# Optimization experiments

Measured on AMD Instinct MI355X. Metric: run time of the kernel, lower is better.

Reference implementation:

```python
import jax, jax.numpy as jnp
import numpy as np

EPS = 1e-7  # keras backend epsilon


def _tril_indices(stack_size: int) -> np.ndarray:
    # matches np.nonzero(np.tri(S, S, -1).ravel())[0] in build()
    return np.nonzero(np.tri(stack_size, stack_size, -1).ravel())[0]


def setup_inputs() -> dict:
    key = jax.random.key(0)
    x = jax.random.normal(key, (8, 512, 256), dtype=jnp.float32)
    return {"x": x}


def reference(x) -> jnp.ndarray:
    B, S, D = x.shape
    tril = jnp.asarray(_tril_indices(S))  # static, length S*(S-1)/2
    # pairwise squared L2 over feature dim: (B, S, S, D) -> (B, S, S)
    diff = x[:, :, None, :] - x[:, None, :, :]
    d2 = jnp.sum(jnp.square(diff), axis=-1)
    d = jnp.sqrt(jnp.maximum(d2, EPS))
    # flatten the S x S matrix and gather strict lower-triangular entries
    out = d.reshape(B, S * S)[:, tril]  # (B, S*(S-1)/2)
    return out
```

## Files before the change

### kernel.cpp

```cpp
#include <hip/hip_runtime.h>
#include <hip/hip_bf16.h>
#include <math.h>

#define BB 8
#define SS 512
#define DD 256
#define PP (SS * (SS - 1) / 2)
#define TILES_PER_B (32 * 33 / 2)

typedef short bf16x8 __attribute__((ext_vector_type(8)));
typedef float f32x4 __attribute__((ext_vector_type(4)));

static __device__ inline unsigned short f2bf(float f) {
    unsigned int u = __float_as_uint(f);
    unsigned int r = u + 0x7fffu + ((u >> 16) & 1u);
    return (unsigned short)(r >> 16);
}

__global__ __launch_bounds__(256) void prep_kernel(const float* __restrict__ x,
                                                   unsigned short* __restrict__ xb,
                                                   float* __restrict__ norms) {
    int row  = blockIdx.x * 4 + (threadIdx.x >> 6);
    int lane = threadIdx.x & 63;
    const float4* src = reinterpret_cast<const float4*>(x + (size_t)row * DD) + lane;
    float4 v = *src;
    float ss = v.x * v.x + v.y * v.y + v.z * v.z + v.w * v.w;
    ushort4 pk;
    pk.x = f2bf(v.x); pk.y = f2bf(v.y); pk.z = f2bf(v.z); pk.w = f2bf(v.w);
    *reinterpret_cast<ushort4*>(xb + (size_t)row * DD + lane * 4) = pk;
    #pragma unroll
    for (int o = 32; o > 0; o >>= 1) ss += __shfl_down(ss, o);
    if (lane == 0) norms[row] = ss;
}

__global__ __launch_bounds__(256) void dist_kernel(const unsigned short* __restrict__ xb,
                                                   const float* __restrict__ norms,
                                                   float* __restrict__ out) {
    int w    = blockIdx.x * 4 + (threadIdx.x >> 6);
    int lane = threadIdx.x & 63;
    int b    = w / TILES_PER_B;
    int tidx = w - b * TILES_PER_B;
    int ti = (int)((sqrtf(8.0f * (float)tidx + 1.0f) - 1.0f) * 0.5f);
    while ((ti + 1) * (ti + 2) / 2 <= tidx) ti++;
    while (ti * (ti + 1) / 2 > tidx) ti--;
    int tj = tidx - ti * (ti + 1) / 2;

    int nidx = lane & 15;
    int quad = lane >> 4;

    const unsigned short* arow = xb + ((size_t)(b * SS + ti * 16 + nidx)) * DD + quad * 8;
    const unsigned short* brow = xb + ((size_t)(b * SS + tj * 16 + nidx)) * DD + quad * 8;

    f32x4 acc = {0.f, 0.f, 0.f, 0.f};
    #pragma unroll
    for (int k = 0; k < DD; k += 32) {
        bf16x8 av = *reinterpret_cast<const bf16x8*>(arow + k);
        bf16x8 bv = *reinterpret_cast<const bf16x8*>(brow + k);
        acc = __builtin_amdgcn_mfma_f32_16x16x32_bf16(av, bv, acc, 0, 0, 0);
    }

    int jg = tj * 16 + nidx;
    float nj = norms[b * SS + jg];
    float* outb = out + (size_t)b * PP;
    #pragma unroll
    for (int r = 0; r < 4; r++) {
        int ig = ti * 16 + quad * 4 + r;
        if (ig > jg) {
            float ni = norms[b * SS + ig];
            float d2 = ni + nj - 2.0f * acc[r];
            d2 = fmaxf(d2, 1e-7f);
            outb[(size_t)(ig * (ig - 1) / 2) + jg] = sqrtf(d2);
        }
    }
}

extern "C" void kernel_launch(void* const* d_in, const int* in_sizes, int n_in,
                              void* d_out, int out_size, void* d_ws, size_t ws_size,
                              hipStream_t stream) {
    const float* x = (const float*)d_in[0];
    float* out = (float*)d_out;
    unsigned short* xb = (unsigned short*)d_ws;
    float* norms = (float*)((char*)d_ws + (size_t)BB * SS * DD * 2);

    prep_kernel<<<1024, 256, 0, stream>>>(x, xb, norms);
    dist_kernel<<<1056, 256, 0, stream>>>(xb, norms, out);
}
```

Before: 68.15 us.

## Fuse bf16 conversion and norm computation into the distance kernel

```diff
diff --git a/kernel.cpp b/kernel.cpp
--- a/kernel.cpp
+++ b/kernel.cpp
@@ -1,5 +1,4 @@
 #include <hip/hip_runtime.h>
-#include <hip/hip_bf16.h>
 #include <math.h>
 
 #define BB 8
@@ -13,62 +12,64 @@
 
 static __device__ inline unsigned short f2bf(float f) {
     unsigned int u = __float_as_uint(f);
-    unsigned int r = u + 0x7fffu + ((u >> 16) & 1u);
-    return (unsigned short)(r >> 16);
+    return (unsigned short)((u + 0x7fffu + ((u >> 16) & 1u)) >> 16);
 }
 
-__global__ __launch_bounds__(256) void prep_kernel(const float* __restrict__ x,
-                                                   unsigned short* __restrict__ xb,
-                                                   float* __restrict__ norms) {
-    int row  = blockIdx.x * 4 + (threadIdx.x >> 6);
-    int lane = threadIdx.x & 63;
-    const float4* src = reinterpret_cast<const float4*>(x + (size_t)row * DD) + lane;
-    float4 v = *src;
-    float ss = v.x * v.x + v.y * v.y + v.z * v.z + v.w * v.w;
-    ushort4 pk;
-    pk.x = f2bf(v.x); pk.y = f2bf(v.y); pk.z = f2bf(v.z); pk.w = f2bf(v.w);
-    *reinterpret_cast<ushort4*>(xb + (size_t)row * DD + lane * 4) = pk;
-    #pragma unroll
-    for (int o = 32; o > 0; o >>= 1) ss += __shfl_down(ss, o);
-    if (lane == 0) norms[row] = ss;
-}
-
-__global__ __launch_bounds__(256) void dist_kernel(const unsigned short* __restrict__ xb,
-                                                   const float* __restrict__ norms,
-                                                   float* __restrict__ out) {
+__global__ __launch_bounds__(256) void dist_fused(const float* __restrict__ x,
+                                                  float* __restrict__ out) {
     int w    = blockIdx.x * 4 + (threadIdx.x >> 6);
     int lane = threadIdx.x & 63;
     int b    = w / TILES_PER_B;
-    int tidx = w - b * TILES_PER_B;
-    int ti = (int)((sqrtf(8.0f * (float)tidx + 1.0f) - 1.0f) * 0.5f);
-    while ((ti + 1) * (ti + 2) / 2 <= tidx) ti++;
-    while (ti * (ti + 1) / 2 > tidx) ti--;
-    int tj = tidx - ti * (ti + 1) / 2;
+    int t    = w - b * TILES_PER_B;
+    int ti = (int)((sqrtf(8.0f * (float)t + 1.0f) - 1.0f) * 0.5f);
+    while ((ti + 1) * (ti + 2) / 2 <= t) ti++;
+    while (ti * (ti + 1) / 2 > t) ti--;
+    int tj = t - ti * (ti + 1) / 2;
 
-    int nidx = lane & 15;
+    int il   = lane & 15;
     int quad = lane >> 4;
 
-    const unsigned short* arow = xb + ((size_t)(b * SS + ti * 16 + nidx)) * DD + quad * 8;
-    const unsigned short* brow = xb + ((size_t)(b * SS + tj * 16 + nidx)) * DD + quad * 8;
+    const float* arow = x + ((size_t)(b * SS + ti * 16 + il)) * DD + quad * 8;
+    const float* brow = x + ((size_t)(b * SS + tj * 16 + il)) * DD + quad * 8;
 
     f32x4 acc = {0.f, 0.f, 0.f, 0.f};
+    float na = 0.f, nb = 0.f;
     #pragma unroll
     for (int k = 0; k < DD; k += 32) {
-        bf16x8 av = *reinterpret_cast<const bf16x8*>(arow + k);
-        bf16x8 bv = *reinterpret_cast<const bf16x8*>(brow + k);
+        float4 a0 = *reinterpret_cast<const float4*>(arow + k);
+        float4 a1 = *reinterpret_cast<const float4*>(arow + k + 4);
+        float4 b0 = *reinterpret_cast<const float4*>(brow + k);
+        float4 b1 = *reinterpret_cast<const float4*>(brow + k + 4);
+
+        na += a0.x*a0.x + a0.y*a0.y + a0.z*a0.z + a0.w*a0.w
+            + a1.x*a1.x + a1.y*a1.y + a1.z*a1.z + a1.w*a1.w;
+        nb += b0.x*b0.x + b0.y*b0.y + b0.z*b0.z + b0.w*b0.w
+            + b1.x*b1.x + b1.y*b1.y + b1.z*b1.z + b1.w*b1.w;
+
+        bf16x8 av, bv;
+        av[0] = (short)f2bf(a0.x); av[1] = (short)f2bf(a0.y);
+        av[2] = (short)f2bf(a0.z); av[3] = (short)f2bf(a0.w);
+        av[4] = (short)f2bf(a1.x); av[5] = (short)f2bf(a1.y);
+        av[6] = (short)f2bf(a1.z); av[7] = (short)f2bf(a1.w);
+        bv[0] = (short)f2bf(b0.x); bv[1] = (short)f2bf(b0.y);
+        bv[2] = (short)f2bf(b0.z); bv[3] = (short)f2bf(b0.w);
+        bv[4] = (short)f2bf(b1.x); bv[5] = (short)f2bf(b1.y);
+        bv[6] = (short)f2bf(b1.z); bv[7] = (short)f2bf(b1.w);
+
         acc = __builtin_amdgcn_mfma_f32_16x16x32_bf16(av, bv, acc, 0, 0, 0);
     }
 
-    int jg = tj * 16 + nidx;
-    float nj = norms[b * SS + jg];
+    na += __shfl_xor(na, 16); na += __shfl_xor(na, 32);
+    nb += __shfl_xor(nb, 16); nb += __shfl_xor(nb, 32);
+
+    int jg = tj * 16 + il;
     float* outb = out + (size_t)b * PP;
     #pragma unroll
     for (int r = 0; r < 4; r++) {
         int ig = ti * 16 + quad * 4 + r;
+        float ni = __shfl(na, quad * 4 + r);
         if (ig > jg) {
-            float ni = norms[b * SS + ig];
-            float d2 = ni + nj - 2.0f * acc[r];
-            d2 = fmaxf(d2, 1e-7f);
+            float d2 = fmaxf(ni + nb - 2.0f * acc[r], 1e-7f);
             outb[(size_t)(ig * (ig - 1) / 2) + jg] = sqrtf(d2);
         }
     }
@@ -79,9 +80,5 @@
                               hipStream_t stream) {
     const float* x = (const float*)d_in[0];
     float* out = (float*)d_out;
-    unsigned short* xb = (unsigned short*)d_ws;
-    float* norms = (float*)((char*)d_ws + (size_t)BB * SS * DD * 2);
-
-    prep_kernel<<<1024, 256, 0, stream>>>(x, xb, norms);
-    dist_kernel<<<1056, 256, 0, stream>>>(xb, norms, out);
+    dist_fused<<<1056, 256, 0, stream>>>(x, out);
 }
```

Measured after the change: 73.68 us. +8.1%, slower.
